# Kernel optimization log

Measured on AMD Instinct MI355X. Metric: run time of the kernel, lower is better.

The kernel has to match this reference:

```python
import jax, jax.numpy as jnp
import numpy as np

N_NODES = 100000
N_EDGES = 1000000
IN_CH, HID_CH, N_CLS = 128, 64, 40


def setup_inputs() -> dict:
    key = jax.random.key(0)
    ks = jax.random.split(key, 8)
    x = jax.random.normal(ks[0], (N_NODES, IN_CH), dtype=jnp.float32)
    edge_index = jax.random.randint(ks[1], (2, N_EDGES), 0, N_NODES, dtype=jnp.int32)
    # Glorot-ish scaled weights (ARMAConv init_weight / root_weight, K=1 stack squeezed)
    w1_init = jax.random.normal(ks[2], (IN_CH, HID_CH), dtype=jnp.float32) / np.sqrt(IN_CH)
    w1_root = jax.random.normal(ks[3], (IN_CH, HID_CH), dtype=jnp.float32) / np.sqrt(IN_CH)
    b1 = jnp.zeros((HID_CH,), dtype=jnp.float32)
    w2_init = jax.random.normal(ks[4], (HID_CH, N_CLS), dtype=jnp.float32) / np.sqrt(HID_CH)
    w2_root = jax.random.normal(ks[5], (HID_CH, N_CLS), dtype=jnp.float32) / np.sqrt(HID_CH)
    b2 = jnp.zeros((N_CLS,), dtype=jnp.float32)
    return {"x": x, "edge_index": edge_index,
            "w1_init": w1_init, "w1_root": w1_root, "b1": b1,
            "w2_init": w2_init, "w2_root": w2_root, "b2": b2}


def _arma_layer(x, row, col, norm, w_init, w_root, bias):
    # ARMAConv, num_stacks=1, num_layers=1, shared_weights=True, eval mode (dropout=id):
    # out = relu( A_hat @ (x W_init) + x W_root + b ), mean over the single stack.
    h = x @ w_init                           # [N, F_out]
    msg = norm[:, None] * h[row]             # gather from source nodes, [E, F_out]
    agg = jax.ops.segment_sum(msg, col, num_segments=N_NODES)  # scatter-add at targets
    return jax.nn.relu(agg + x @ w_root + bias)


def reference(x, edge_index, w1_init, w1_root, b1, w2_init, w2_root, b2):
    row, col = edge_index[0], edge_index[1]
    # gcn_norm, add_self_loops=False: deg over targets, norm = d^-1/2[row] * d^-1/2[col]
    deg = jax.ops.segment_sum(jnp.ones((row.shape[0],), x.dtype), col, num_segments=N_NODES)
    dinv = jnp.where(deg > 0, jax.lax.rsqrt(jnp.maximum(deg, 1e-12)), jnp.zeros_like(deg))
    norm = dinv[row] * dinv[col]
    h = _arma_layer(x, row, col, norm, w1_init, w1_root, b1)
    h = jax.nn.relu(h)  # BiARMA relu; dropout identity in eval
    return _arma_layer(h, row, col, norm, w2_init, w2_root, b2)
```

## Files before the change

### kernel.cpp

```cpp
#include <hip/hip_runtime.h>

#define N_NODES 100000
#define N_EDGES 1000000
#define IN_CH 128
#define HID_CH 64
#define N_CLS 40

#define NBUCK 782

static inline int cdiv(int a, int b) { return (a + b - 1) / b; }

using bf16x8 = __attribute__((ext_vector_type(8))) short;
using f32x4  = __attribute__((ext_vector_type(4))) float;

__device__ __forceinline__ unsigned pack_bf2(float a, float b) {
    unsigned ua = __float_as_uint(a), ub = __float_as_uint(b);
    ua += 0x7fffu + ((ua >> 16) & 1u);
    ub += 0x7fffu + ((ub >> 16) & 1u);
    return (ua >> 16) | (ub & 0xffff0000u);
}
__device__ __forceinline__ unsigned short bf16_of(float a) {
    unsigned ua = __float_as_uint(a);
    ua += 0x7fffu + ((ua >> 16) & 1u);
    return (unsigned short)(ua >> 16);
}
__device__ __forceinline__ float bf_lo(unsigned u) { return __uint_as_float(u << 16); }
__device__ __forceinline__ float bf_hi(unsigned u) { return __uint_as_float(u & 0xffff0000u); }


__global__ __launch_bounds__(256)
void bucket_count_kernel(const int* __restrict__ cols, int* __restrict__ gcount, int E) {
    __shared__ int hist[NBUCK];
    for (int i = threadIdx.x; i < NBUCK; i += 256) hist[i] = 0;
    __syncthreads();
    int per = (E + gridDim.x - 1) / gridDim.x;
    int s = blockIdx.x * per;
    int e = min(E, s + per);
    for (int j = s + threadIdx.x; j < e; j += 256)
        atomicAdd(&hist[cols[j] >> 7], 1);
    __syncthreads();
    for (int i = threadIdx.x; i < NBUCK; i += 256)
        if (hist[i]) atomicAdd(&gcount[i], hist[i]);
}


__global__ __launch_bounds__(1024)
void scan_bucket_kernel(const int* __restrict__ gcount, int* __restrict__ boff,
                        int* __restrict__ gcursor, int* __restrict__ offsets) {
    __shared__ int part[1024];
    int t = threadIdx.x;
    part[t] = (t < NBUCK) ? gcount[t] : 0;
    __syncthreads();
    for (int off = 1; off < 1024; off <<= 1) {
        int v = (t >= off) ? part[t - off] : 0;
        __syncthreads();
        part[t] += v;
        __syncthreads();
    }
    int excl = (t > 0) ? part[t - 1] : 0;
    if (t < NBUCK) { boff[t] = excl; gcursor[t] = excl; }
    if (t == NBUCK) { boff[NBUCK] = excl; offsets[N_NODES] = excl; }
}


__global__ __launch_bounds__(256)
void bucket_scatter_kernel(const int* __restrict__ rows, const int* __restrict__ cols,
                           int* __restrict__ gcursor, int* __restrict__ pedge, int E) {
    __shared__ int cur[NBUCK];
    for (int i = threadIdx.x; i < NBUCK; i += 256) cur[i] = 0;
    __syncthreads();
    int per = (E + gridDim.x - 1) / gridDim.x;
    int s = blockIdx.x * per;
    int e = min(E, s + per);
    for (int j = s + threadIdx.x; j < e; j += 256)
        atomicAdd(&cur[cols[j] >> 7], 1);
    __syncthreads();
    for (int i = threadIdx.x; i < NBUCK; i += 256) {
        int h = cur[i];
        cur[i] = h ? atomicAdd(&gcursor[i], h) : 0;
    }
    __syncthreads();
    for (int j = s + threadIdx.x; j < e; j += 256) {
        int c = cols[j];
        int pos = atomicAdd(&cur[c >> 7], 1);
        pedge[pos] = (rows[j] << 7) | (c & 127);
    }
}


__global__ __launch_bounds__(256)
void bucket_sort_kernel(const int* __restrict__ boff, const int* __restrict__ pedge,
                        int* __restrict__ srow, int* __restrict__ offsets,
                        float* __restrict__ dinv) {
    __shared__ int cnt[128];
    __shared__ int scn[128];
    __shared__ int cur[128];
    int b = blockIdx.x, t = threadIdx.x;
    if (t < 128) cnt[t] = 0;
    __syncthreads();
    int e0 = boff[b], e1 = boff[b + 1];
    for (int j = e0 + t; j < e1; j += 256)
        atomicAdd(&cnt[pedge[j] & 127], 1);
    __syncthreads();
    if (t < 128) scn[t] = cnt[t];
    __syncthreads();
    for (int off = 1; off < 128; off <<= 1) {
        int v = 0;
        if (t < 128 && t >= off) v = scn[t - off];
        __syncthreads();
        if (t < 128) scn[t] += v;
        __syncthreads();
    }
    if (t < 128) {
        int excl = (t > 0) ? scn[t - 1] : 0;
        cur[t] = excl;
        int node = b * 128 + t;
        if (node < N_NODES) {
            offsets[node] = e0 + excl;
            dinv[node] = cnt[t] ? rsqrtf((float)cnt[t]) : 0.f;
        }
    }
    __syncthreads();
    for (int j = e0 + t; j < e1; j += 256) {
        int p = pedge[j];
        int pos = atomicAdd(&cur[p & 127], 1);
        srow[e0 + pos] = p >> 7;
    }
}


__global__ __launch_bounds__(256)
void wconv_kernel(const float* __restrict__ w1i, const float* __restrict__ w1r,
                  const float* __restrict__ w2i, const float* __restrict__ w2r,
                  unsigned* __restrict__ wtgA, unsigned* __restrict__ wtgB) {
    int id = blockIdx.x * 256 + threadIdx.x;
    if (id < 128 * 64) {
        int c = id >> 6, kp = id & 63;
        int k = kp * 2;
        const float* W = (c < 64) ? w1i : w1r;
        int cc = (c < 64) ? c : c - 64;
        float a = W[(size_t)k * 64 + cc];
        float b = W[(size_t)(k + 1) * 64 + cc];
        wtgA[c * 64 + kp] = pack_bf2(a, b);
    } else if (id < 128 * 64 + 80 * 32) {
        int j = id - 128 * 64;
        int c = j >> 5, kp = j & 31;
        int k = kp * 2;
        const float* W = (c < 40) ? w2i : w2r;
        int cc = (c < 40) ? c : c - 40;
        float a = W[(size_t)k * 40 + cc];
        float b = W[(size_t)(k + 1) * 40 + cc];
        wtgB[c * 32 + kp] = pack_bf2(a, b);
    }
}


template<int K, int C1, int C2>
__launch_bounds__(256, 4)
__global__ void gemm_mfma_direct_kernel(const float* __restrict__ X,
                                        const unsigned short* __restrict__ WT,
                                        const float* __restrict__ Bias,
                                        const float* __restrict__ dinv,
                                        unsigned short* __restrict__ Y1b,
                                        float* __restrict__ Y2, int N) {
    constexpr int CT = C1 + C2;
    constexpr int NT = CT / 16;
    constexpr int KS = K / 32;
    static_assert(CT % 16 == 0 && K % 32 == 0, "shape");

    const int tid = threadIdx.x;
    const int wave = tid >> 6;
    const int lane = tid & 63;
    const int m = lane & 15;
    const int quad = lane >> 4;
    const int r0 = blockIdx.x * 64;
    const int rowbase = wave * 16;

    const int rowA = r0 + rowbase + m;
    const bool va = (rowA < N);
    const float* xrow = X + (size_t)rowA * K + quad * 8;
    float4 xv[KS][2];
#pragma unroll
    for (int ks = 0; ks < KS; ++ks) {
        if (va) {
            xv[ks][0] = *reinterpret_cast<const float4*>(xrow + ks * 32);
            xv[ks][1] = *reinterpret_cast<const float4*>(xrow + ks * 32 + 4);
        } else {
            xv[ks][0] = make_float4(0.f, 0.f, 0.f, 0.f);
            xv[ks][1] = make_float4(0.f, 0.f, 0.f, 0.f);
        }
    }

    union AFrag { uint4 u; bf16x8 v; };
    AFrag af[KS];
#pragma unroll
    for (int ks = 0; ks < KS; ++ks) {
        af[ks].u.x = pack_bf2(xv[ks][0].x, xv[ks][0].y);
        af[ks].u.y = pack_bf2(xv[ks][0].z, xv[ks][0].w);
        af[ks].u.z = pack_bf2(xv[ks][1].x, xv[ks][1].y);
        af[ks].u.w = pack_bf2(xv[ks][1].z, xv[ks][1].w);
    }

    f32x4 acc[NT];
#pragma unroll
    for (int t = 0; t < NT; ++t) acc[t] = (f32x4){0.f, 0.f, 0.f, 0.f};

#pragma unroll
    for (int ks = 0; ks < KS; ++ks) {
        bf16x8 a = af[ks].v;
#pragma unroll
        for (int t = 0; t < NT; ++t) {
            bf16x8 b = *reinterpret_cast<const bf16x8*>(&WT[(size_t)(t * 16 + m) * K + ks * 32 + quad * 8]);
            acc[t] = __builtin_amdgcn_mfma_f32_16x16x32_bf16(a, b, acc[t], 0, 0, 0);
        }
    }

    const int rbase = r0 + rowbase + quad * 4;
    float dv[4];
#pragma unroll
    for (int reg = 0; reg < 4; ++reg)
        dv[reg] = (rbase + reg < N) ? dinv[rbase + reg] : 0.f;

#pragma unroll
    for (int t = 0; t < NT; ++t) {
        int c = t * 16 + m;
        float bias = (c >= C1) ? Bias[c - C1] : 0.f;
#pragma unroll
        for (int reg = 0; reg < 4; ++reg) {
            int r = rbase + reg;
            if (r >= N) continue;
            float v = acc[t][reg];
            if (c < C1) {
                Y1b[(size_t)r * C1 + c] = bf16_of(v * dv[reg]);
            } else {
                Y2[(size_t)r * C2 + (c - C1)] = v + bias;
            }
        }
    }
}


template<int K, int C1, int C2>
__launch_bounds__(256)
__global__ void gemm_mfma_fused_kernel(const float* __restrict__ X,
                                       const float* __restrict__ W1,
                                       const float* __restrict__ W2,
                                       const float* __restrict__ Bias,
                                       const float* __restrict__ dinv,
                                       unsigned short* __restrict__ Y1b,
                                       float* __restrict__ Y2, int N) {
    constexpr int CT = C1 + C2;
    constexpr int NT = CT / 16;
    constexpr int KS = K / 32;
    constexpr int KP = (K + 8) / 2;
    static_assert(CT % 16 == 0 && K % 32 == 0, "shape");
    static_assert(C1 % 4 == 0 && C2 % 4 == 0, "staging vec4");

    __shared__ unsigned xb[64 * KP];
    __shared__ unsigned wt[CT * KP];
    __shared__ float dloc[64];

    const int tid = threadIdx.x;
    const int wave = tid >> 6;
    const int lane = tid & 63;
    const int m = lane & 15;
    const int quad = lane >> 4;
    const int r0 = blockIdx.x * 64;

    if (tid < 64) {
        int gr = r0 + tid;
        dloc[tid] = (gr < N) ? dinv[gr] : 0.f;
    }

    constexpr int XIT = 64 * (K / 4);
    for (int i = tid; i < XIT; i += 256) {
        int rr = i / (K / 4);
        int k4 = i - rr * (K / 4);
        int gr = r0 + rr;
        float4 v = make_float4(0.f, 0.f, 0.f, 0.f);
        if (gr < N)
            v = *reinterpret_cast<const float4*>(&X[(size_t)gr * K + k4 * 4]);
        uint2 p;
        p.x = pack_bf2(v.x, v.y);
        p.y = pack_bf2(v.z, v.w);
        *reinterpret_cast<uint2*>(&xb[rr * KP + k4 * 2]) = p;
    }

    constexpr int WIT = (K / 2) * (CT / 4);
    for (int i = tid; i < WIT; i += 256) {
        int kp = i / (CT / 4);
        int c4 = i - kp * (CT / 4);
        int k = kp * 2;
        int c = c4 * 4;
        float4 va, vb;
        if (c < C1) {
            va = *reinterpret_cast<const float4*>(&W1[(size_t)k * C1 + c]);
            vb = *reinterpret_cast<const float4*>(&W1[(size_t)(k + 1) * C1 + c]);
        } else {
            va = *reinterpret_cast<const float4*>(&W2[(size_t)k * C2 + (c - C1)]);
            vb = *reinterpret_cast<const float4*>(&W2[(size_t)(k + 1) * C2 + (c - C1)]);
        }
        wt[(c + 0) * KP + kp] = pack_bf2(va.x, vb.x);
        wt[(c + 1) * KP + kp] = pack_bf2(va.y, vb.y);
        wt[(c + 2) * KP + kp] = pack_bf2(va.z, vb.z);
        wt[(c + 3) * KP + kp] = pack_bf2(va.w, vb.w);
    }
    __syncthreads();

    const int rowbase = wave * 16;
    f32x4 acc[NT];
#pragma unroll
    for (int t = 0; t < NT; ++t) acc[t] = (f32x4){0.f, 0.f, 0.f, 0.f};

#pragma unroll
    for (int ks = 0; ks < KS; ++ks) {
        bf16x8 a = *reinterpret_cast<const bf16x8*>(&xb[(rowbase + m) * KP + ks * 16 + quad * 4]);
#pragma unroll
        for (int t = 0; t < NT; ++t) {
            bf16x8 b = *reinterpret_cast<const bf16x8*>(&wt[(t * 16 + m) * KP + ks * 16 + quad * 4]);
            acc[t] = __builtin_amdgcn_mfma_f32_16x16x32_bf16(a, b, acc[t], 0, 0, 0);
        }
    }

#pragma unroll
    for (int t = 0; t < NT; ++t) {
        int c = t * 16 + m;
        float bias = (c >= C1) ? Bias[c - C1] : 0.f;
#pragma unroll
        for (int reg = 0; reg < 4; ++reg) {
            int rl = rowbase + quad * 4 + reg;
            int r = r0 + rl;
            if (r >= N) continue;
            float v = acc[t][reg];
            if (c < C1) {
                Y1b[(size_t)r * C1 + c] = bf16_of(v * dloc[rl]);
            } else {
                Y2[(size_t)r * C2 + (c - C1)] = v + bias;
            }
        }
    }
}


template<int C>
__launch_bounds__(256)
__global__ void pull_bf16_kernel(const int* __restrict__ offsets,
                                 const int* __restrict__ srow,
                                 const float* __restrict__ dinv,
                                 const unsigned* __restrict__ H,
                                 float* __restrict__ Y, int N) {
    constexpr int TPE = C / 4;
    constexpr int CH = C / 2;
    int gid = blockIdx.x * blockDim.x + threadIdx.x;
    int node = gid / TPE;
    int lane = gid - node * TPE;
    if (node >= N) return;

    int e0 = offsets[node];
    int e1 = offsets[node + 1];
    float dc = dinv[node];

    float4 acc = make_float4(0.f, 0.f, 0.f, 0.f);
    int j = e0;
    for (; j + 4 <= e1; j += 4) {
        int r0 = srow[j + 0];
        int r1 = srow[j + 1];
        int r2 = srow[j + 2];
        int r3 = srow[j + 3];
        uint2 u0 = *reinterpret_cast<const uint2*>(&H[(size_t)r0 * CH + lane * 2]);
        uint2 u1 = *reinterpret_cast<const uint2*>(&H[(size_t)r1 * CH + lane * 2]);
        uint2 u2 = *reinterpret_cast<const uint2*>(&H[(size_t)r2 * CH + lane * 2]);
        uint2 u3 = *reinterpret_cast<const uint2*>(&H[(size_t)r3 * CH + lane * 2]);
        acc.x += (bf_lo(u0.x) + bf_lo(u1.x)) + (bf_lo(u2.x) + bf_lo(u3.x));
        acc.y += (bf_hi(u0.x) + bf_hi(u1.x)) + (bf_hi(u2.x) + bf_hi(u3.x));
        acc.z += (bf_lo(u0.y) + bf_lo(u1.y)) + (bf_lo(u2.y) + bf_lo(u3.y));
        acc.w += (bf_hi(u0.y) + bf_hi(u1.y)) + (bf_hi(u2.y) + bf_hi(u3.y));
    }
    for (; j < e1; ++j) {
        int r = srow[j];
        uint2 u = *reinterpret_cast<const uint2*>(&H[(size_t)r * CH + lane * 2]);
        acc.x += bf_lo(u.x);
        acc.y += bf_hi(u.x);
        acc.z += bf_lo(u.y);
        acc.w += bf_hi(u.y);
    }

    float4* Y4 = reinterpret_cast<float4*>(Y);
    size_t yi = (size_t)node * TPE + lane;
    float4 y = Y4[yi];
    y.x = fmaxf(fmaf(dc, acc.x, y.x), 0.f);
    y.y = fmaxf(fmaf(dc, acc.y, y.y), 0.f);
    y.z = fmaxf(fmaf(dc, acc.z, y.z), 0.f);
    y.w = fmaxf(fmaf(dc, acc.w, y.w), 0.f);
    Y4[yi] = y;
}


extern "C" void kernel_launch(void* const* d_in, const int* in_sizes, int n_in,
                              void* d_out, int out_size, void* d_ws, size_t ws_size,
                              hipStream_t stream) {
    const float* x       = (const float*)d_in[0];
    const int*   eidx    = (const int*)d_in[1];
    const float* w1_init = (const float*)d_in[2];
    const float* w1_root = (const float*)d_in[3];
    const float* b1      = (const float*)d_in[4];
    const float* w2_init = (const float*)d_in[5];
    const float* w2_root = (const float*)d_in[6];
    const float* b2      = (const float*)d_in[7];
    float* out = (float*)d_out;

    const int* rows = eidx;
    const int* cols = eidx + N_EDGES;

    int* wsi = (int*)d_ws;
    int*      gcount  = wsi;
    int*      boff    = wsi + 784;
    int*      gcursor = wsi + 1572;
    float*    dinv    = (float*)(wsi + 2360);
    int*      offsets = wsi + 102360;
    int*      srow    = wsi + 202364;
    unsigned* h0b     = (unsigned*)(wsi + 1202364);
    int*      pedge   = wsi + 1202364;
    float*    agg1    = (float*)(wsi + 4402364);
    unsigned* h2b     = h0b;
    unsigned* wtgA    = (unsigned*)(wsi + 10802364);
    unsigned* wtgB    = wtgA + 8192;
    const size_t WS_NEEDED = 10813116ull * 4ull;

    hipMemsetAsync(gcount, 0, 784 * sizeof(int), stream);
    bucket_count_kernel<<<128, 256, 0, stream>>>(cols, gcount, N_EDGES);
    scan_bucket_kernel<<<1, 1024, 0, stream>>>(gcount, boff, gcursor, offsets);
    bucket_scatter_kernel<<<128, 256, 0, stream>>>(rows, cols, gcursor, pedge, N_EDGES);
    bucket_sort_kernel<<<NBUCK, 256, 0, stream>>>(boff, pedge, srow, offsets, dinv);

    const int GGRID = cdiv(N_NODES, 64);

    if (ws_size >= WS_NEEDED) {
        wconv_kernel<<<42, 256, 0, stream>>>(w1_init, w1_root, w2_init, w2_root, wtgA, wtgB);

        gemm_mfma_direct_kernel<IN_CH, HID_CH, HID_CH><<<GGRID, 256, 0, stream>>>(
            x, (const unsigned short*)wtgA, b1, dinv, (unsigned short*)h0b, agg1, N_NODES);
        pull_bf16_kernel<HID_CH><<<cdiv(N_NODES * (HID_CH / 4), 256), 256, 0, stream>>>(
            offsets, srow, dinv, h0b, agg1, N_NODES);

        gemm_mfma_direct_kernel<HID_CH, N_CLS, N_CLS><<<GGRID, 256, 0, stream>>>(
            agg1, (const unsigned short*)wtgB, b2, dinv, (unsigned short*)h2b, out, N_NODES);
        pull_bf16_kernel<N_CLS><<<cdiv(N_NODES * (N_CLS / 4), 256), 256, 0, stream>>>(
            offsets, srow, dinv, h2b, out, N_NODES);
    } else {
        gemm_mfma_fused_kernel<IN_CH, HID_CH, HID_CH><<<GGRID, 256, 0, stream>>>(
            x, w1_init, w1_root, b1, dinv, (unsigned short*)h0b, agg1, N_NODES);
        pull_bf16_kernel<HID_CH><<<cdiv(N_NODES * (HID_CH / 4), 256), 256, 0, stream>>>(
            offsets, srow, dinv, h0b, agg1, N_NODES);
        gemm_mfma_fused_kernel<HID_CH, N_CLS, N_CLS><<<GGRID, 256, 0, stream>>>(
            agg1, w2_init, w2_root, b2, dinv, (unsigned short*)h2b, out, N_NODES);
        pull_bf16_kernel<N_CLS><<<cdiv(N_NODES * (N_CLS / 4), 256), 256, 0, stream>>>(
            offsets, srow, dinv, h2b, out, N_NODES);
    }
}
```

Before: 273.7 us.

## Make GEMM kernels persistent with weights staged once in padded LDS

Replaces the one-tile-per-block GEMM with a persistent kernel on a fixed grid of 1024 blocks that loops over 64-row tiles. Each block loads the bf16 transposed weights into shared memory once, with padding to avoid bank conflicts, and hoists the bias loads out of the tile loop. This removes repeated global weight fetches per tile. In exchange it adds LDS usage that may limit occupancy and drops the overlap that came from many short-lived blocks.

```diff
diff --git a/kernel.cpp b/kernel.cpp
--- a/kernel.cpp
+++ b/kernel.cpp
@@ -7,6 +7,7 @@
 #define N_CLS 40
 
 #define NBUCK 782
+#define GEMM_GRID 1024
 
 static inline int cdiv(int a, int b) { return (a + b - 1) / b; }
 
@@ -157,83 +158,94 @@
 
 template<int K, int C1, int C2>
 __launch_bounds__(256, 4)
-__global__ void gemm_mfma_direct_kernel(const float* __restrict__ X,
-                                        const unsigned short* __restrict__ WT,
-                                        const float* __restrict__ Bias,
-                                        const float* __restrict__ dinv,
-                                        unsigned short* __restrict__ Y1b,
-                                        float* __restrict__ Y2, int N) {
+__global__ void gemm_persist_kernel(const float* __restrict__ X,
+                                    const unsigned short* __restrict__ WT,
+                                    const float* __restrict__ Bias,
+                                    const float* __restrict__ dinv,
+                                    unsigned short* __restrict__ Y1b,
+                                    float* __restrict__ Y2, int N, int ntiles) {
     constexpr int CT = C1 + C2;
     constexpr int NT = CT / 16;
     constexpr int KS = K / 32;
+    constexpr int KP = K / 2 + 4;
     static_assert(CT % 16 == 0 && K % 32 == 0, "shape");
+
+    __shared__ unsigned wt[CT * KP];
 
     const int tid = threadIdx.x;
     const int wave = tid >> 6;
     const int lane = tid & 63;
     const int m = lane & 15;
     const int quad = lane >> 4;
-    const int r0 = blockIdx.x * 64;
-    const int rowbase = wave * 16;
-
-    const int rowA = r0 + rowbase + m;
-    const bool va = (rowA < N);
-    const float* xrow = X + (size_t)rowA * K + quad * 8;
-    float4 xv[KS][2];
-#pragma unroll
-    for (int ks = 0; ks < KS; ++ks) {
-        if (va) {
-            xv[ks][0] = *reinterpret_cast<const float4*>(xrow + ks * 32);
-            xv[ks][1] = *reinterpret_cast<const float4*>(xrow + ks * 32 + 4);
-        } else {
-            xv[ks][0] = make_float4(0.f, 0.f, 0.f, 0.f);
-            xv[ks][1] = make_float4(0.f, 0.f, 0.f, 0.f);
-        }
-    }
-
-    union AFrag { uint4 u; bf16x8 v; };
-    AFrag af[KS];
-#pragma unroll
-    for (int ks = 0; ks < KS; ++ks) {
-        af[ks].u.x = pack_bf2(xv[ks][0].x, xv[ks][0].y);
-        af[ks].u.y = pack_bf2(xv[ks][0].z, xv[ks][0].w);
-        af[ks].u.z = pack_bf2(xv[ks][1].x, xv[ks][1].y);
-        af[ks].u.w = pack_bf2(xv[ks][1].z, xv[ks][1].w);
-    }
-
-    f32x4 acc[NT];
-#pragma unroll
-    for (int t = 0; t < NT; ++t) acc[t] = (f32x4){0.f, 0.f, 0.f, 0.f};
-
-#pragma unroll
-    for (int ks = 0; ks < KS; ++ks) {
-        bf16x8 a = af[ks].v;
-#pragma unroll
-        for (int t = 0; t < NT; ++t) {
-            bf16x8 b = *reinterpret_cast<const bf16x8*>(&WT[(size_t)(t * 16 + m) * K + ks * 32 + quad * 8]);
-            acc[t] = __builtin_amdgcn_mfma_f32_16x16x32_bf16(a, b, acc[t], 0, 0, 0);
-        }
-    }
-
-    const int rbase = r0 + rowbase + quad * 4;
-    float dv[4];
-#pragma unroll
-    for (int reg = 0; reg < 4; ++reg)
-        dv[reg] = (rbase + reg < N) ? dinv[rbase + reg] : 0.f;
-
+
+    constexpr int WDW = CT * (K / 2);
+    const unsigned* wtg = (const unsigned*)WT;
+    for (int i = tid * 4; i < WDW; i += 256 * 4) {
+        int c = i / (K / 2);
+        int j = i - c * (K / 2);
+        uint4 v = *reinterpret_cast<const uint4*>(wtg + i);
+        *reinterpret_cast<uint4*>(&wt[c * KP + j]) = v;
+    }
+    __syncthreads();
+
+    float biasv[NT];
 #pragma unroll
     for (int t = 0; t < NT; ++t) {
         int c = t * 16 + m;
-        float bias = (c >= C1) ? Bias[c - C1] : 0.f;
-#pragma unroll
-        for (int reg = 0; reg < 4; ++reg) {
-            int r = rbase + reg;
-            if (r >= N) continue;
-            float v = acc[t][reg];
-            if (c < C1) {
-                Y1b[(size_t)r * C1 + c] = bf16_of(v * dv[reg]);
-            } else {
-                Y2[(size_t)r * C2 + (c - C1)] = v + bias;
+        biasv[t] = (c >= C1) ? Bias[c - C1] : 0.f;
+    }
+
+    for (int tile = blockIdx.x; tile < ntiles; tile += gridDim.x) {
+        const int rowA = tile * 64 + wave * 16 + m;
+        const bool va = (rowA < N);
+        const float* xr = X + (size_t)rowA * K + quad * 8;
+
+        union AFrag { uint4 u; bf16x8 v; } af[KS];
+#pragma unroll
+        for (int ks = 0; ks < KS; ++ks) {
+            float4 v0 = make_float4(0.f, 0.f, 0.f, 0.f);
+            float4 v1 = make_float4(0.f, 0.f, 0.f, 0.f);
+            if (va) {
+                v0 = *reinterpret_cast<const float4*>(xr + ks * 32);
+                v1 = *reinterpret_cast<const float4*>(xr + ks * 32 + 4);
+            }
+            af[ks].u.x = pack_bf2(v0.x, v0.y);
+            af[ks].u.y = pack_bf2(v0.z, v0.w);
+            af[ks].u.z = pack_bf2(v1.x, v1.y);
+            af[ks].u.w = pack_bf2(v1.z, v1.w);
+        }
+
+        f32x4 acc[NT];
+#pragma unroll
+        for (int t = 0; t < NT; ++t) acc[t] = (f32x4){0.f, 0.f, 0.f, 0.f};
+#pragma unroll
+        for (int ks = 0; ks < KS; ++ks) {
+#pragma unroll
+            for (int t = 0; t < NT; ++t) {
+                bf16x8 b = *reinterpret_cast<const bf16x8*>(&wt[(t * 16 + m) * KP + ks * 16 + quad * 4]);
+                acc[t] = __builtin_amdgcn_mfma_f32_16x16x32_bf16(af[ks].v, b, acc[t], 0, 0, 0);
+            }
+        }
+
+        const int rbase = tile * 64 + wave * 16 + quad * 4;
+        float dv[4];
+#pragma unroll
+        for (int reg = 0; reg < 4; ++reg)
+            dv[reg] = (rbase + reg < N) ? dinv[rbase + reg] : 0.f;
+
+#pragma unroll
+        for (int t = 0; t < NT; ++t) {
+            int c = t * 16 + m;
+#pragma unroll
+            for (int reg = 0; reg < 4; ++reg) {
+                int r = rbase + reg;
+                if (r >= N) continue;
+                float v = acc[t][reg];
+                if (c < C1) {
+                    Y1b[(size_t)r * C1 + c] = bf16_of(v * dv[reg]);
+                } else {
+                    Y2[(size_t)r * C2 + (c - C1)] = v + biasv[t];
+                }
             }
         }
     }
@@ -433,26 +445,28 @@
     bucket_scatter_kernel<<<128, 256, 0, stream>>>(rows, cols, gcursor, pedge, N_EDGES);
     bucket_sort_kernel<<<NBUCK, 256, 0, stream>>>(boff, pedge, srow, offsets, dinv);
 
-    const int GGRID = cdiv(N_NODES, 64);
+    const int NTILES = cdiv(N_NODES, 64);
 
     if (ws_size >= WS_NEEDED) {
         wconv_kernel<<<42, 256, 0, stream>>>(w1_init, w1_root, w2_init, w2_root, wtgA, wtgB);
 
-        gemm_mfma_direct_kernel<IN_CH, HID_CH, HID_CH><<<GGRID, 256, 0, stream>>>(
-            x, (const unsigned short*)wtgA, b1, dinv, (unsigned short*)h0b, agg1, N_NODES);
+        gemm_persist_kernel<IN_CH, HID_CH, HID_CH><<<GEMM_GRID, 256, 0, stream>>>(
+            x, (const unsigned short*)wtgA, b1, dinv, (unsigned short*)h0b, agg1,
+            N_NODES, NTILES);
         pull_bf16_kernel<HID_CH><<<cdiv(N_NODES * (HID_CH / 4), 256), 256, 0, stream>>>(
             offsets, srow, dinv, h0b, agg1, N_NODES);
 
-        gemm_mfma_direct_kernel<HID_CH, N_CLS, N_CLS><<<GGRID, 256, 0, stream>>>(
-            agg1, (const unsigned short*)wtgB, b2, dinv, (unsigned short*)h2b, out, N_NODES);
+        gemm_persist_kernel<HID_CH, N_CLS, N_CLS><<<GEMM_GRID, 256, 0, stream>>>(
+            agg1, (const unsigned short*)wtgB, b2, dinv, (unsigned short*)h2b, out,
+            N_NODES, NTILES);
         pull_bf16_kernel<N_CLS><<<cdiv(N_NODES * (N_CLS / 4), 256), 256, 0, stream>>>(
             offsets, srow, dinv, h2b, out, N_NODES);
     } else {
-        gemm_mfma_fused_kernel<IN_CH, HID_CH, HID_CH><<<GGRID, 256, 0, stream>>>(
+        gemm_mfma_fused_kernel<IN_CH, HID_CH, HID_CH><<<NTILES, 256, 0, stream>>>(
             x, w1_init, w1_root, b1, dinv, (unsigned short*)h0b, agg1, N_NODES);
         pull_bf16_kernel<HID_CH><<<cdiv(N_NODES * (HID_CH / 4), 256), 256, 0, stream>>>(
             offsets, srow, dinv, h0b, agg1, N_NODES);
-        gemm_mfma_fused_kernel<HID_CH, N_CLS, N_CLS><<<GGRID, 256, 0, stream>>>(
+        gemm_mfma_fused_kernel<HID_CH, N_CLS, N_CLS><<<NTILES, 256, 0, stream>>>(
             agg1, w2_init, w2_root, b2, dinv, (unsigned short*)h2b, out, N_NODES);
         pull_bf16_kernel<N_CLS><<<cdiv(N_NODES * (N_CLS / 4), 256), 256, 0, stream>>>(
             offsets, srow, dinv, h2b, out, N_NODES);
```

Result: slower. 282.0 us (+3.0%).
